# Performance work log

Hardware: AMD Instinct MI355X
Metric: run time of the kernel (lower is better)

Reference implementation:

```python
import math
import jax, jax.numpy as jnp
import numpy as np

B, S, D, H = 2, 2048, 2048, 16
HD = D // H  # head_dim = 128


def setup_inputs() -> dict:
    key = jax.random.key(0)
    ks = jax.random.split(key, 5)
    x = jax.random.normal(ks[0], (B, S, D), dtype=jnp.float32)
    # torch nn.Linear weights are [out_features, in_features]
    wq = jax.random.normal(ks[1], (D, D), dtype=jnp.float32) * 0.02
    wk = jax.random.normal(ks[2], (D, D), dtype=jnp.float32) * 0.02
    wv = jax.random.normal(ks[3], (D, D), dtype=jnp.float32) * 0.02
    wo = jax.random.normal(ks[4], (D, D), dtype=jnp.float32) * 0.02
    # llama-style rotary frequencies: freq_cis[t, i] = exp(1j * t / 10000^(2i/hd))
    inv_freq = 1.0 / (10000.0 ** (jnp.arange(0, HD, 2, dtype=jnp.float32) / HD))  # [HD/2]
    angles = jnp.arange(S, dtype=jnp.float32)[:, None] * inv_freq[None, :]  # [S, HD/2]
    freq_cos = jnp.cos(angles)
    freq_sin = jnp.sin(angles)
    # additive causal mask (0 on/below diagonal, large negative above)
    mask = jnp.triu(jnp.full((S, S), -1e9, dtype=jnp.float32), k=1)
    return {"x": x, "wq": wq, "wk": wk, "wv": wv, "wo": wo,
            "freq_cos": freq_cos, "freq_sin": freq_sin, "mask": mask}


def _rope(t, cos, sin):
    # t: [B, H, S, HD]; cos/sin: [S, HD/2]. Consecutive pairs form complex numbers.
    b, h, s, hd = t.shape
    tr = t.reshape(b, h, s, hd // 2, 2)
    re, im = tr[..., 0], tr[..., 1]
    c = cos[None, None, :, :]
    sn = sin[None, None, :, :]
    out_re = re * c - im * sn
    out_im = re * sn + im * c
    return jnp.stack([out_re, out_im], axis=-1).reshape(b, h, s, hd)


def reference(x, wq, wk, wv, wo, freq_cos, freq_sin, mask):
    b, s, d = x.shape
    hd = 2 * freq_cos.shape[-1]
    h = wq.shape[0] // hd
    # projections (torch Linear: y = x @ W.T)
    q = jnp.einsum('bsd,ed->bse', x, wq).reshape(b, s, h, hd).transpose(0, 2, 1, 3)
    k = jnp.einsum('bsd,ed->bse', x, wk).reshape(b, s, h, hd).transpose(0, 2, 1, 3)
    v = jnp.einsum('bsd,ed->bse', x, wv).reshape(b, s, h, hd).transpose(0, 2, 1, 3)
    q = _rope(q, freq_cos, freq_sin)
    k = _rope(k, freq_cos, freq_sin)
    scores = jnp.einsum('bhqd,bhkd->bhqk', q, k) / math.sqrt(hd)  # [B,H,S,S]
    scores = scores + mask[None, None, :, :]
    attn = jax.nn.softmax(scores, axis=-1)
    o = jnp.einsum('bhqk,bhkd->bhqd', attn, v)
    o = o.transpose(0, 2, 1, 3).reshape(b, s, h * hd)
    return jnp.einsum('bse,de->bsd', o, wo)
```

## Files before the change

### kernel.cpp

```cpp
#include <hip/hip_runtime.h>
#include <stdint.h>

#define BB  2
#define SS  2048
#define DD  2048
#define HH  16
#define HDD 128
#define MM  (BB * SS)

typedef __attribute__((ext_vector_type(8)))  short short8;
typedef __attribute__((ext_vector_type(4)))  float f32x4;
typedef __attribute__((ext_vector_type(16))) float f32x16;
typedef unsigned int   u32;
typedef unsigned short u16;
typedef __attribute__((ext_vector_type(4))) u16 u16x4;
typedef __attribute__((ext_vector_type(2))) u32 u32x2;
typedef __attribute__((ext_vector_type(4))) u32 u32x4;

static __device__ __forceinline__ u16 f2bf(float f) {
  u32 u = __builtin_bit_cast(u32, f);
  u32 r = u + 0x7fffu + ((u >> 16) & 1u);
  return (u16)(r >> 16);
}

static __device__ __forceinline__ u32 cvtpk(float a, float b) {
  u32 r;
  asm("v_cvt_pk_bf16_f32 %0, %1, %2" : "=v"(r) : "v"(a), "v"(b));
  return r;
}
static __device__ __forceinline__ void permswap(u32& a, u32& b) {
  asm volatile("v_permlane32_swap_b32 %0, %1" : "+v"(a), "+v"(b));
}

__global__ void cvt_all(const float* __restrict__ x,  const float* __restrict__ wq,
                        const float* __restrict__ wk, const float* __restrict__ wv,
                        const float* __restrict__ wo,
                        u16* __restrict__ xb, u16* __restrict__ wqkv,
                        u16* __restrict__ wob) {
  const int NX = (MM * DD) / 4;
  const int NW = (DD * DD) / 4;
  int i = blockIdx.x * blockDim.x + threadIdx.x;
  const float* s; u16* d; int off;
  if (i < NX) { s = x; d = xb; off = i; }
  else {
    int j = i - NX; int w = j >> 20; off = j & (NW - 1);
    s = (w == 0) ? wq : (w == 1) ? wk : (w == 2) ? wv : wo;
    d = (w < 3) ? (wqkv + (size_t)w * DD * DD) : wob;
  }
  f32x4 v = *(const f32x4*)(s + (size_t)off * 4);
  u16x4 o;
#pragma unroll
  for (int j = 0; j < 4; ++j) o[j] = f2bf(v[j]);
  *(u16x4*)(d + (size_t)off * 4) = o;
}

template <int MODE>
__global__ __launch_bounds__(256) void gemm2(const u16* __restrict__ A,
                                             const u16* __restrict__ Bw,
                                             u16* __restrict__ Cq,
                                             u16* __restrict__ Ck,
                                             u16* __restrict__ Cvt,
                                             float* __restrict__ Cf,
                                             int M, int N, int K,
                                             const float* __restrict__ fc,
                                             const float* __restrict__ fs) {
  __shared__ __align__(16) u16 Al[3][128 * 32];
  __shared__ __align__(16) u16 Bl[3][128 * 32];
  const int tid  = threadIdx.x;
  const int wave = tid >> 6, lane = tid & 63;
  const int m0 = blockIdx.y * 128, n0 = blockIdx.x * 128;
  const int wr = (wave >> 1) * 64, wc = (wave & 1) * 64;
  const int lrow = lane & 15, lk = (lane >> 4) * 8;

  f32x4 acc[4][4] = {};

#define GSTAGE(T, BUF)                                                                  \
  {                                                                                     \
    int koff = (T) * 32;                                                                \
    _Pragma("unroll")                                                                   \
    for (int i_ = 0; i_ < 2; ++i_) {                                                    \
      int idx = tid + i_ * 256;                                                         \
      int row = idx >> 2, kc = (idx & 3) * 8;                                           \
      const u16* ga = A  + (size_t)(m0 + row) * K + koff + kc;                          \
      const u16* gb = Bw + (size_t)(n0 + row) * K + koff + kc;                          \
      __builtin_amdgcn_global_load_lds((const __attribute__((address_space(1))) u32*)ga,\
                                       (__attribute__((address_space(3))) u32*)(&Al[BUF][0] + idx * 8), \
                                       16, 0, 0);                                       \
      __builtin_amdgcn_global_load_lds((const __attribute__((address_space(1))) u32*)gb,\
                                       (__attribute__((address_space(3))) u32*)(&Bl[BUF][0] + idx * 8), \
                                       16, 0, 0);                                       \
    }                                                                                   \
  }

  const int NT = K / 32;
  GSTAGE(0, 0);
  int cur = 0;
  for (int t = 0; t < NT; ++t) {
    int nxt = cur + 1; if (nxt == 3) nxt = 0;
    if (t + 1 < NT) {
      GSTAGE(t + 1, nxt);
      asm volatile("s_waitcnt vmcnt(4)" ::: "memory");
    } else {
      asm volatile("s_waitcnt vmcnt(0)" ::: "memory");
    }
    __builtin_amdgcn_s_barrier();

    const u16* Ab = &Al[cur][0];
    const u16* Bb = &Bl[cur][0];
    short8 af[4], bfr[4];
#pragma unroll
    for (int tt = 0; tt < 4; ++tt) {
      af[tt]  = *(const short8*)(Ab + (wr + tt * 16 + lrow) * 32 + lk);
      bfr[tt] = *(const short8*)(Bb + (wc + tt * 16 + lrow) * 32 + lk);
    }
#pragma unroll
    for (int mt = 0; mt < 4; ++mt)
#pragma unroll
      for (int nt = 0; nt < 4; ++nt)
        acc[mt][nt] = __builtin_amdgcn_mfma_f32_16x16x32_bf16(af[mt], bfr[nt], acc[mt][nt], 0, 0, 0);
    cur = nxt;
  }
#undef GSTAGE

  const int dr = (lane >> 4) * 4;
  if constexpr (MODE == 1) {
#pragma unroll
    for (int mt = 0; mt < 4; ++mt)
#pragma unroll
      for (int nt = 0; nt < 4; ++nt)
#pragma unroll
        for (int i = 0; i < 4; ++i) {
          size_t r = (size_t)(m0 + wr + mt * 16 + dr + i);
          size_t c = (size_t)(n0 + wc + nt * 16 + lrow);
          Cf[r * N + c] = acc[mt][nt][i];
        }
  } else {
    const int region = n0 >> 11;
    if (region < 2) {
      u16* Cd = region ? Ck : Cq;
      const float sfac = region ? 1.f : 0.08838834764831845f * 1.44269504088896340736f;
#pragma unroll
      for (int mt = 0; mt < 4; ++mt)
#pragma unroll
        for (int nt = 0; nt < 4; ++nt) {
          int c  = n0 + wc + nt * 16 + lrow;
          int cl = c & 2047;
          int dh = cl & 127, pi = dh >> 1;
          float sgn = (dh & 1) ? 1.f : -1.f;
#pragma unroll
          for (int i = 0; i < 4; ++i) {
            int r  = m0 + wr + mt * 16 + dr + i;
            int s_ = r & (SS - 1);
            float cc_ = fc[s_ * 64 + pi] * sfac;
            float ss_ = fs[s_ * 64 + pi] * (sgn * sfac);
            float v  = acc[mt][nt][i];
            float pv = __shfl_xor(v, 1, 64);
            Cd[(size_t)r * 2048 + cl] = f2bf(v * cc_ + pv * ss_);
          }
        }
    } else {
#pragma unroll
      for (int mt = 0; mt < 4; ++mt)
#pragma unroll
        for (int nt = 0; nt < 4; ++nt) {
          int cl = (n0 - 4096) + wc + nt * 16 + lrow;
          int rr = m0 + wr + mt * 16 + dr;
          int b  = rr >> 11, s0 = rr & 2047;
          u16x4 pk;
#pragma unroll
          for (int i = 0; i < 4; ++i) pk[i] = f2bf(acc[mt][nt][i]);
          *(u16x4*)(Cvt + ((size_t)b * 2048 + cl) * 2048 + s0) = pk;
        }
    }
  }
}

__global__ __launch_bounds__(256, 2) void attn_kernel(const u16* __restrict__ Q,
                                                      const u16* __restrict__ K,
                                                      const u16* __restrict__ Vt,
                                                      u16* __restrict__ O) {
  __shared__ __align__(16) u16 Kl[2][64 * 128];
  __shared__ __align__(16) u16 Vl[2][128 * 64];

  const int tid = threadIdx.x, wave = tid >> 6, lane = tid & 63;
  const int l31 = lane & 31, hi = lane >> 5;
  const int bh = blockIdx.x, b = bh >> 4, h = bh & 15;
  const int y = blockIdx.y;
  const int qt = (y < 8) ? y : (23 - y);
  const size_t base    = ((size_t)b * SS) * DD + (size_t)h * HDD;
  const size_t vt_base = (size_t)bh * HDD * SS;
  const int swz = (l31 & 7) << 4;

#define STAGE(KT, BUF)                                                              \
  {                                                                                 \
    int k0s = (KT) * 64;                                                            \
    _Pragma("unroll")                                                               \
    for (int i_ = 0; i_ < 4; ++i_) {                                                \
      int idx = tid + i_ * 256;                                                     \
      int kr = idx >> 4, c_ = idx & 15;                                             \
      const u16* gk = K + base + (size_t)(k0s + kr) * DD + ((c_ ^ (kr & 7)) * 8);   \
      __builtin_amdgcn_global_load_lds((const __attribute__((address_space(1))) u32*)gk, \
                                       (__attribute__((address_space(3))) u32*)(&Kl[BUF][0] + idx * 8), \
                                       16, 0, 0);                                   \
      int dv = idx >> 3, c2 = idx & 7;                                              \
      const u16* gv = Vt + vt_base + (size_t)dv * SS + k0s + ((c2 ^ (dv & 7)) * 8); \
      __builtin_amdgcn_global_load_lds((const __attribute__((address_space(1))) u32*)gv, \
                                       (__attribute__((address_space(3))) u32*)(&Vl[BUF][0] + idx * 8), \
                                       16, 0, 0);                                   \
    }                                                                               \
  }

  const int qw = qt * 128 + wave * 32;
  const int q_ = qw + l31;

  short8 qf[8];
#pragma unroll
  for (int kc = 0; kc < 8; ++kc)
    qf[kc] = *(const short8*)(Q + base + (size_t)(qw + l31) * DD + kc * 16 + hi * 8);

  f32x16 oacc[4] = {};
  float m_i = -1e30f, l_p = 0.f;

  int buf = 0;
  STAGE(0, 0);

  const int ntiles = 2 * qt + 2;
  for (int kt = 0; kt < ntiles; ++kt) {
    const int k0 = kt * 64;
    if (kt + 1 < ntiles) {
      STAGE(kt + 1, buf ^ 1);
      asm volatile("s_waitcnt vmcnt(8)" ::: "memory");
    } else {
      asm volatile("s_waitcnt vmcnt(0)" ::: "memory");
    }
    __builtin_amdgcn_s_barrier();

    if (k0 <= qw + 31) {
      const u16* Kb_ = &Kl[buf][0];
      const u16* Vb_ = &Vl[buf][0];

      f32x16 st[2] = {};
      __builtin_amdgcn_s_setprio(1);
#pragma unroll
      for (int kc = 0; kc < 8; ++kc) {
        int by0 = (l31 * 256)        + ((kc * 32 + hi * 16) ^ swz);
        int by1 = ((32 + l31) * 256) + ((kc * 32 + hi * 16) ^ swz);
        short8 a0 = *(const short8*)(Kb_ + (by0 >> 1));
        short8 a1 = *(const short8*)(Kb_ + (by1 >> 1));
        st[0] = __builtin_amdgcn_mfma_f32_32x32x16_bf16(a0, qf[kc], st[0], 0, 0, 0);
        st[1] = __builtin_amdgcn_mfma_f32_32x32x16_bf16(a1, qf[kc], st[1], 0, 0, 0);
      }
      __builtin_amdgcn_s_setprio(0);

      float mx = -1e30f;
      if (k0 + 63 > qw) {
#pragma unroll
        for (int kb = 0; kb < 2; ++kb)
#pragma unroll
          for (int r = 0; r < 16; ++r) {
            float s = st[kb][r];
            int key = k0 + kb * 32 + (r & 3) + ((r >> 2) << 3) + (hi << 2);
            if (key > q_) s = -1e30f;
            st[kb][r] = s;
            mx = fmaxf(mx, s);
          }
      } else {
#pragma unroll
        for (int kb = 0; kb < 2; ++kb)
#pragma unroll
          for (int r = 0; r < 16; ++r) mx = fmaxf(mx, st[kb][r]);
      }
      mx = fmaxf(mx, __shfl_xor(mx, 32, 64));

      if (__any(mx > m_i + 8.f)) {
        float mn  = fmaxf(m_i, mx);
        float esc = exp2f(m_i - mn);
        m_i = mn; l_p *= esc;
#pragma unroll
        for (int db = 0; db < 4; ++db)
#pragma unroll
          for (int r = 0; r < 16; ++r) oacc[db][r] *= esc;
      }
      float sum = 0.f;
#pragma unroll
      for (int kb = 0; kb < 2; ++kb)
#pragma unroll
        for (int r = 0; r < 16; ++r) {
          float e = exp2f(st[kb][r] - m_i);
          st[kb][r] = e;
          sum += e;
        }
      l_p += sum;

      __builtin_amdgcn_s_setprio(1);
#pragma unroll
      for (int kb = 0; kb < 2; ++kb) {
#pragma unroll
        for (int half = 0; half < 2; ++half) {
          const int rb = half * 8;
          u32 w0 = cvtpk(st[kb][rb + 0], st[kb][rb + 1]);
          u32 w1 = cvtpk(st[kb][rb + 2], st[kb][rb + 3]);
          u32 w2 = cvtpk(st[kb][rb + 4], st[kb][rb + 5]);
          u32 w3 = cvtpk(st[kb][rb + 6], st[kb][rb + 7]);
          permswap(w0, w2);
          permswap(w1, w3);
          short8 pf = __builtin_bit_cast(short8, (u32x4){w0, w1, w2, w3});
          const int ktv = kb * 2 + half;
#pragma unroll
          for (int db = 0; db < 4; ++db) {
            int d = db * 32 + l31;
            int by = d * 128 + ((ktv * 32 + hi * 16) ^ swz);
            short8 vf = *(const short8*)(Vb_ + (by >> 1));
            oacc[db] = __builtin_amdgcn_mfma_f32_32x32x16_bf16(vf, pf, oacc[db], 0, 0, 0);
          }
        }
      }
      __builtin_amdgcn_s_setprio(0);
    }
    __builtin_amdgcn_s_barrier();
    buf ^= 1;
  }

  float lt  = l_p + __shfl_xor(l_p, 32, 64);
  float inv = 1.f / lt;
#pragma unroll
  for (int db = 0; db < 4; ++db)
#pragma unroll
    for (int g = 0; g < 4; ++g) {
      int d0 = db * 32 + 8 * g + 4 * hi;
      u32x2 pk;
      pk[0] = cvtpk(oacc[db][4 * g + 0] * inv, oacc[db][4 * g + 1] * inv);
      pk[1] = cvtpk(oacc[db][4 * g + 2] * inv, oacc[db][4 * g + 3] * inv);
      *(u32x2*)(O + base + (size_t)q_ * DD + d0) = pk;
    }
#undef STAGE
}

extern "C" void kernel_launch(void* const* d_in, const int* in_sizes, int n_in,
                              void* d_out, int out_size, void* d_ws, size_t ws_size,
                              hipStream_t stream) {
  (void)in_sizes; (void)n_in; (void)out_size; (void)ws_size;
  const float* x  = (const float*)d_in[0];
  const float* wq = (const float*)d_in[1];
  const float* wk = (const float*)d_in[2];
  const float* wv = (const float*)d_in[3];
  const float* wo = (const float*)d_in[4];
  const float* fc = (const float*)d_in[5];
  const float* fs = (const float*)d_in[6];
  float* out = (float*)d_out;

  const size_t XBUF = (size_t)MM * DD * 2;
  const size_t WBUF = (size_t)DD * DD * 2;
  char* ws = (char*)d_ws;
  u16* xb   = (u16*)(ws);
  u16* Qb   = (u16*)(ws + XBUF);
  u16* Kb   = (u16*)(ws + 2 * XBUF);
  u16* Vtb  = (u16*)(ws + 3 * XBUF);
  u16* wqkv = (u16*)(ws + 4 * XBUF);
  u16* wob  = (u16*)(ws + 4 * XBUF + 3 * WBUF);
  u16* Ob   = xb;

  const int ncv = (MM * DD) / 4 + 4 * ((DD * DD) / 4);
  cvt_all<<<ncv / 256, 256, 0, stream>>>(x, wq, wk, wv, wo, xb, wqkv, wob);

  gemm2<4><<<dim3(48, 32), 256, 0, stream>>>(xb, wqkv, Qb, Kb, Vtb, nullptr,
                                             MM, 3 * DD, DD, fc, fs);

  attn_kernel<<<dim3(32, 16), 256, 0, stream>>>(Qb, Kb, Vtb, Ob);

  gemm2<1><<<dim3(16, 32), 256, 0, stream>>>(Ob, wob, nullptr, nullptr, nullptr, out,
                                             MM, DD, DD, nullptr, nullptr);
}
```

Baseline: 267.1 us.

## Replace QKV GEMM with 256x256-tile 8-wave kernel using direct global-to-LDS loads

Result: slower. 277.2 us (+3.8%).

```diff
diff --git a/kernel.cpp b/kernel.cpp
--- a/kernel.cpp
+++ b/kernel.cpp
@@ -54,16 +54,142 @@
   *(u16x4*)(d + (size_t)off * 4) = o;
 }
 
-template <int MODE>
-__global__ __launch_bounds__(256) void gemm2(const u16* __restrict__ A,
-                                             const u16* __restrict__ Bw,
-                                             u16* __restrict__ Cq,
-                                             u16* __restrict__ Ck,
-                                             u16* __restrict__ Cvt,
-                                             float* __restrict__ Cf,
-                                             int M, int N, int K,
-                                             const float* __restrict__ fc,
-                                             const float* __restrict__ fs) {
+__global__ __launch_bounds__(512, 2) void gemm8_qkv(const u16* __restrict__ A,
+                                                    const u16* __restrict__ Bw,
+                                                    u16* __restrict__ Cq,
+                                                    u16* __restrict__ Ck,
+                                                    u16* __restrict__ Cvt,
+                                                    const float* __restrict__ fc,
+                                                    const float* __restrict__ fs) {
+  const int K = DD;
+  __shared__ __align__(16) u16 Al[2][256 * 64];
+  __shared__ __align__(16) u16 Bl[2][256 * 64];
+  const int tid = threadIdx.x, lane = tid & 63;
+  const int wid = tid >> 6;
+  const int wm = wid >> 2, wn = wid & 3;
+  const int m0b = blockIdx.y * 256, n0b = blockIdx.x * 256;
+  const int lrow = lane & 15, kh = lane >> 4;
+  const int sk = lrow & 7;
+
+  f32x4 acc[8][4] = {};
+
+#define STG(Tt, BUF) do {                                                             \
+    int k0s = (Tt) * 64;                                                              \
+    _Pragma("unroll")                                                                 \
+    for (int j_ = 0; j_ < 4; ++j_) {                                                  \
+      int i_ = tid + j_ * 512;                                                        \
+      int r_ = i_ >> 3, c_ = i_ & 7;                                                  \
+      int sc_ = (c_ ^ (r_ & 7)) * 8;                                                  \
+      const u16* ga = A + (size_t)(m0b + r_) * K + k0s + sc_;                         \
+      __builtin_amdgcn_global_load_lds((const __attribute__((address_space(1))) u32*)ga, \
+          (__attribute__((address_space(3))) u32*)(&Al[BUF][0] + i_ * 8), 16, 0, 0);  \
+      const u16* gb = Bw + (size_t)(n0b + r_) * K + k0s + sc_;                        \
+      __builtin_amdgcn_global_load_lds((const __attribute__((address_space(1))) u32*)gb, \
+          (__attribute__((address_space(3))) u32*)(&Bl[BUF][0] + i_ * 8), 16, 0, 0);  \
+    } } while (0)
+
+#define RDA(MH)                                                                       \
+    _Pragma("unroll")                                                                 \
+    for (int f = 0; f < 4; ++f)                                                       \
+      _Pragma("unroll")                                                               \
+      for (int ks = 0; ks < 2; ++ks)                                                  \
+        a[f][ks] = *(const short8*)(Ab + ((MH) * 64 + f * 16 + lrow) * 64             \
+                                       + (((ks * 4 + kh) ^ sk) * 8));
+
+#define RDB(NH)                                                                       \
+    _Pragma("unroll")                                                                 \
+    for (int g = 0; g < 2; ++g)                                                       \
+      _Pragma("unroll")                                                               \
+      for (int ks = 0; ks < 2; ++ks)                                                  \
+        b[g][ks] = *(const short8*)(Bb + ((NH) * 32 + g * 16 + lrow) * 64             \
+                                       + (((ks * 4 + kh) ^ sk) * 8));
+
+#define QUAD(MH, NH)                                                                  \
+    __builtin_amdgcn_s_setprio(1);                                                    \
+    _Pragma("unroll")                                                                 \
+    for (int f = 0; f < 4; ++f)                                                       \
+      _Pragma("unroll")                                                               \
+      for (int g = 0; g < 2; ++g)                                                     \
+        _Pragma("unroll")                                                             \
+        for (int ks = 0; ks < 2; ++ks)                                                \
+          acc[(MH) * 4 + f][(NH) * 2 + g] = __builtin_amdgcn_mfma_f32_16x16x32_bf16(  \
+              a[f][ks], b[g][ks], acc[(MH) * 4 + f][(NH) * 2 + g], 0, 0, 0);          \
+    __builtin_amdgcn_s_setprio(0);
+
+  STG(0, 0);
+
+  const int NT = K / 64;
+  for (int t = 0; t < NT; ++t) {
+    const int bt = t & 1;
+    __builtin_amdgcn_s_barrier();
+    __builtin_amdgcn_sched_barrier(0);
+    if (t + 1 < NT) {
+      STG(t + 1, bt ^ 1);
+      asm volatile("s_waitcnt vmcnt(8)" ::: "memory");
+    } else {
+      asm volatile("s_waitcnt vmcnt(0)" ::: "memory");
+    }
+    __builtin_amdgcn_s_barrier();
+    __builtin_amdgcn_sched_barrier(0);
+
+    const u16* Ab = &Al[bt][0] + wm * (128 * 64);
+    const u16* Bb = &Bl[bt][0] + wn * (64 * 64);
+    short8 a[4][2], b[2][2];
+
+    RDA(0); RDB(0); QUAD(0, 0);
+    RDB(1);         QUAD(0, 1);
+    RDA(1);         QUAD(1, 1);
+    RDB(0);         QUAD(1, 0);
+  }
+#undef STG
+#undef RDA
+#undef RDB
+#undef QUAD
+
+  const int dr = kh * 4;
+  const int region = n0b >> 11;
+  if (region < 2) {
+    u16* Cd = region ? Ck : Cq;
+    const float sfac = region ? 1.f : 0.08838834764831845f * 1.44269504088896340736f;
+#pragma unroll
+    for (int mf = 0; mf < 8; ++mf)
+#pragma unroll
+      for (int nf = 0; nf < 4; ++nf) {
+        int c  = n0b + wn * 64 + nf * 16 + lrow;
+        int cl = c & 2047;
+        int dh = cl & 127, pi = dh >> 1;
+        float sgn = (dh & 1) ? 1.f : -1.f;
+#pragma unroll
+        for (int i = 0; i < 4; ++i) {
+          int r  = m0b + wm * 128 + mf * 16 + dr + i;
+          int s_ = r & (SS - 1);
+          float cc_ = fc[s_ * 64 + pi] * sfac;
+          float ss_ = fs[s_ * 64 + pi] * (sgn * sfac);
+          float v  = acc[mf][nf][i];
+          float pv = __shfl_xor(v, 1, 64);
+          Cd[(size_t)r * 2048 + cl] = f2bf(v * cc_ + pv * ss_);
+        }
+      }
+  } else {
+#pragma unroll
+    for (int mf = 0; mf < 8; ++mf)
+#pragma unroll
+      for (int nf = 0; nf < 4; ++nf) {
+        int cl = (n0b - 4096) + wn * 64 + nf * 16 + lrow;
+        int rr = m0b + wm * 128 + mf * 16 + dr;
+        int b_ = rr >> 11, s0 = rr & 2047;
+        u16x4 pk;
+#pragma unroll
+        for (int i = 0; i < 4; ++i) pk[i] = f2bf(acc[mf][nf][i]);
+        *(u16x4*)(Cvt + ((size_t)b_ * 2048 + cl) * 2048 + s0) = pk;
+      }
+  }
+}
+
+__global__ __launch_bounds__(256) void gemm_o(const u16* __restrict__ A,
+                                              const u16* __restrict__ Bw,
+                                              float* __restrict__ Cf,
+                                              int M, int N, int K) {
   __shared__ __align__(16) u16 Al[3][128 * 32];
   __shared__ __align__(16) u16 Bl[3][128 * 32];
   const int tid  = threadIdx.x;
@@ -123,56 +249,16 @@
 #undef GSTAGE
 
   const int dr = (lane >> 4) * 4;
-  if constexpr (MODE == 1) {
-#pragma unroll
-    for (int mt = 0; mt < 4; ++mt)
-#pragma unroll
-      for (int nt = 0; nt < 4; ++nt)
-#pragma unroll
-        for (int i = 0; i < 4; ++i) {
-          size_t r = (size_t)(m0 + wr + mt * 16 + dr + i);
-          size_t c = (size_t)(n0 + wc + nt * 16 + lrow);
-          Cf[r * N + c] = acc[mt][nt][i];
-        }
-  } else {
-    const int region = n0 >> 11;
-    if (region < 2) {
-      u16* Cd = region ? Ck : Cq;
-      const float sfac = region ? 1.f : 0.08838834764831845f * 1.44269504088896340736f;
-#pragma unroll
-      for (int mt = 0; mt < 4; ++mt)
-#pragma unroll
-        for (int nt = 0; nt < 4; ++nt) {
-          int c  = n0 + wc + nt * 16 + lrow;
-          int cl = c & 2047;
-          int dh = cl & 127, pi = dh >> 1;
-          float sgn = (dh & 1) ? 1.f : -1.f;
-#pragma unroll
-          for (int i = 0; i < 4; ++i) {
-            int r  = m0 + wr + mt * 16 + dr + i;
-            int s_ = r & (SS - 1);
-            float cc_ = fc[s_ * 64 + pi] * sfac;
-            float ss_ = fs[s_ * 64 + pi] * (sgn * sfac);
-            float v  = acc[mt][nt][i];
-            float pv = __shfl_xor(v, 1, 64);
-            Cd[(size_t)r * 2048 + cl] = f2bf(v * cc_ + pv * ss_);
-          }
-        }
-    } else {
-#pragma unroll
-      for (int mt = 0; mt < 4; ++mt)
-#pragma unroll
-        for (int nt = 0; nt < 4; ++nt) {
-          int cl = (n0 - 4096) + wc + nt * 16 + lrow;
-          int rr = m0 + wr + mt * 16 + dr;
-          int b  = rr >> 11, s0 = rr & 2047;
-          u16x4 pk;
-#pragma unroll
-          for (int i = 0; i < 4; ++i) pk[i] = f2bf(acc[mt][nt][i]);
-          *(u16x4*)(Cvt + ((size_t)b * 2048 + cl) * 2048 + s0) = pk;
-        }
-    }
-  }
+#pragma unroll
+  for (int mt = 0; mt < 4; ++mt)
+#pragma unroll
+    for (int nt = 0; nt < 4; ++nt)
+#pragma unroll
+      for (int i = 0; i < 4; ++i) {
+        size_t r = (size_t)(m0 + wr + mt * 16 + dr + i);
+        size_t c = (size_t)(n0 + wc + nt * 16 + lrow);
+        Cf[r * N + c] = acc[mt][nt][i];
+      }
 }
 
 __global__ __launch_bounds__(256, 2) void attn_kernel(const u16* __restrict__ Q,
@@ -363,11 +449,9 @@
   const int ncv = (MM * DD) / 4 + 4 * ((DD * DD) / 4);
   cvt_all<<<ncv / 256, 256, 0, stream>>>(x, wq, wk, wv, wo, xb, wqkv, wob);
 
-  gemm2<4><<<dim3(48, 32), 256, 0, stream>>>(xb, wqkv, Qb, Kb, Vtb, nullptr,
-                                             MM, 3 * DD, DD, fc, fs);
+  gemm8_qkv<<<dim3(24, 16), 512, 0, stream>>>(xb, wqkv, Qb, Kb, Vtb, fc, fs);
 
   attn_kernel<<<dim3(32, 16), 256, 0, stream>>>(Qb, Kb, Vtb, Ob);
 
-  gemm2<1><<<dim3(16, 32), 256, 0, stream>>>(Ob, wob, nullptr, nullptr, nullptr, out,
-                                             MM, DD, DD, nullptr, nullptr);
-}
+  gemm_o<<<dim3(16, 32), 256, 0, stream>>>(Ob, wob, out, MM, DD, DD);
+}
```

## Double K tile to 64 with XOR-swizzled LDS layout in GEMM

Applied to the files above, without the earlier changes.

After: 247.8 us. 1.08x faster.

```diff
diff --git a/kernel.cpp b/kernel.cpp
--- a/kernel.cpp
+++ b/kernel.cpp
@@ -64,65 +64,71 @@
                                              int M, int N, int K,
                                              const float* __restrict__ fc,
                                              const float* __restrict__ fs) {
-  __shared__ __align__(16) u16 Al[3][128 * 32];
-  __shared__ __align__(16) u16 Bl[3][128 * 32];
+  __shared__ __align__(16) u16 Al[2][128 * 64];
+  __shared__ __align__(16) u16 Bl[2][128 * 64];
   const int tid  = threadIdx.x;
   const int wave = tid >> 6, lane = tid & 63;
   const int m0 = blockIdx.y * 128, n0 = blockIdx.x * 128;
   const int wr = (wave >> 1) * 64, wc = (wave & 1) * 64;
-  const int lrow = lane & 15, lk = (lane >> 4) * 8;
+  const int lrow = lane & 15, kh = lane >> 4;
+  const int sk = lrow & 7;
 
   f32x4 acc[4][4] = {};
 
 #define GSTAGE(T, BUF)                                                                  \
   {                                                                                     \
-    int koff = (T) * 32;                                                                \
+    int koff = (T) * 64;                                                                \
     _Pragma("unroll")                                                                   \
-    for (int i_ = 0; i_ < 2; ++i_) {                                                    \
-      int idx = tid + i_ * 256;                                                         \
-      int row = idx >> 2, kc = (idx & 3) * 8;                                           \
-      const u16* ga = A  + (size_t)(m0 + row) * K + koff + kc;                          \
-      const u16* gb = Bw + (size_t)(n0 + row) * K + koff + kc;                          \
+    for (int j_ = 0; j_ < 4; ++j_) {                                                    \
+      int i_ = tid + j_ * 256;                                             \
+      int r_ = i_ >> 3, c_ = i_ & 7;                                                    \
+      int sc_ = (c_ ^ (r_ & 7)) * 8;                                                    \
+      const u16* ga = A  + (size_t)(m0 + r_) * K + koff + sc_;                          \
       __builtin_amdgcn_global_load_lds((const __attribute__((address_space(1))) u32*)ga,\
-                                       (__attribute__((address_space(3))) u32*)(&Al[BUF][0] + idx * 8), \
+                                       (__attribute__((address_space(3))) u32*)(&Al[BUF][0] + i_ * 8), \
                                        16, 0, 0);                                       \
+      const u16* gb = Bw + (size_t)(n0 + r_) * K + koff + sc_;                          \
       __builtin_amdgcn_global_load_lds((const __attribute__((address_space(1))) u32*)gb,\
-                                       (__attribute__((address_space(3))) u32*)(&Bl[BUF][0] + idx * 8), \
+                                       (__attribute__((address_space(3))) u32*)(&Bl[BUF][0] + i_ * 8), \
                                        16, 0, 0);                                       \
     }                                                                                   \
   }
 
-  const int NT = K / 32;
+  const int NT = K / 64;
   GSTAGE(0, 0);
-  int cur = 0;
   for (int t = 0; t < NT; ++t) {
-    int nxt = cur + 1; if (nxt == 3) nxt = 0;
+    const int bt = t & 1;
     if (t + 1 < NT) {
-      GSTAGE(t + 1, nxt);
-      asm volatile("s_waitcnt vmcnt(4)" ::: "memory");
+      GSTAGE(t + 1, bt ^ 1);
+      asm volatile("s_waitcnt vmcnt(8)" ::: "memory");
     } else {
       asm volatile("s_waitcnt vmcnt(0)" ::: "memory");
     }
     __builtin_amdgcn_s_barrier();
 
-    const u16* Ab = &Al[cur][0];
-    const u16* Bb = &Bl[cur][0];
-    short8 af[4], bfr[4];
-#pragma unroll
-    for (int tt = 0; tt < 4; ++tt) {
-      af[tt]  = *(const short8*)(Ab + (wr + tt * 16 + lrow) * 32 + lk);
-      bfr[tt] = *(const short8*)(Bb + (wc + tt * 16 + lrow) * 32 + lk);
-    }
+    const u16* Ab = &Al[bt][0];
+    const u16* Bb = &Bl[bt][0];
+    short8 af[4][2], bf[4][2];
+#pragma unroll
+    for (int tt = 0; tt < 4; ++tt)
+#pragma unroll
+      for (int ks = 0; ks < 2; ++ks) {
+        af[tt][ks] = *(const short8*)(Ab + (wr + tt * 16 + lrow) * 64 + ((ks * 4 + kh) ^ sk) * 8);
+        bf[tt][ks] = *(const short8*)(Bb + (wc + tt * 16 + lrow) * 64 + ((ks * 4 + kh) ^ sk) * 8);
+      }
 #pragma unroll
     for (int mt = 0; mt < 4; ++mt)
 #pragma unroll
       for (int nt = 0; nt < 4; ++nt)
-        acc[mt][nt] = __builtin_amdgcn_mfma_f32_16x16x32_bf16(af[mt], bfr[nt], acc[mt][nt], 0, 0, 0);
-    cur = nxt;
+#pragma unroll
+        for (int ks = 0; ks < 2; ++ks)
+          acc[mt][nt] = __builtin_amdgcn_mfma_f32_16x16x32_bf16(af[mt][ks], bf[nt][ks], acc[mt][nt], 0, 0, 0);
+
+    __builtin_amdgcn_s_barrier();
   }
 #undef GSTAGE
 
-  const int dr = (lane >> 4) * 4;
+  const int dr = kh * 4;
   if constexpr (MODE == 1) {
 #pragma unroll
     for (int mt = 0; mt < 4; ++mt)
```
